# Performance work log

Hardware: AMD Instinct MI355X
Metric: run time of the kernel (lower is better)

Reference implementation:

```python
import jax, jax.numpy as jnp
import numpy as np

V, E, H, B, S, C = 50000, 300, 512, 128, 80, 6
HH = 2 * H  # hidden_dim * num_directions (BiDi=True)


def _gru_dir(x, w_ih, w_hh, b_ih, b_hh, reverse):
    # x: (b, t, e) -> (b, t, h); torch nn.GRU cell math
    Bv, T, _ = x.shape
    Hd = w_hh.shape[1]
    xg = jnp.einsum('bte,ge->btg', x, w_ih) + b_ih  # (b, t, 3h)
    if reverse:
        xg = xg[:, ::-1]
    def step(h, xt):
        gi_r, gi_z, gi_n = jnp.split(xt, 3, axis=-1)
        gh_r, gh_z, gh_n = jnp.split(h @ w_hh.T + b_hh, 3, axis=-1)
        r = jax.nn.sigmoid(gi_r + gh_r)
        z = jax.nn.sigmoid(gi_z + gh_z)
        n = jnp.tanh(gi_n + r * gh_n)
        hn = (1.0 - z) * n + z * h
        return hn, hn
    h0 = jnp.zeros((Bv, Hd), x.dtype)
    _, hs = jax.lax.scan(step, h0, jnp.swapaxes(xg, 0, 1))
    hs = jnp.swapaxes(hs, 0, 1)
    if reverse:
        hs = hs[:, ::-1]
    return hs


def _bigru(x, pf, pb):
    return jnp.concatenate([_gru_dir(x, *pf, reverse=False), _gru_dir(x, *pb, reverse=True)], axis=-1)


def _conv1d(x, w, b, d):
    y = jax.lax.conv_general_dilated(x, w, (1,), 'VALID', rhs_dilation=(d,),
                                     dimension_numbers=('NCH', 'OIH', 'NCH'))
    return y + b[None, :, None]


def _bn(x, g, b, m, v):
    # eval-mode BatchNorm1d with running stats
    return (x - m[None, :, None]) * (g[None, :, None] / jnp.sqrt(v[None, :, None] + 1e-5)) + b[None, :, None]


def setup_inputs():
    key = jax.random.key(0)
    ks = iter(jax.random.split(key, 64))
    def W(*shape):
        return jax.random.normal(next(ks), shape, jnp.float32) * 0.02
    inp = {
        'input_batch': jax.random.randint(next(ks), (B, S), 1, V),
        'choices_batch': jax.random.randint(next(ks), (B, 4, C), 1, V),
        'emb_table': W(V, E),
    }
    for p in ('sg', 'cg'):
        for d in ('f', 'b'):
            inp[p + '_wih_' + d] = W(3 * H, E)
            inp[p + '_whh_' + d] = W(3 * H, H)
            inp[p + '_bih_' + d] = W(3 * H)
            inp[p + '_bhh_' + d] = W(3 * H)
    inp['lin_w'] = W(HH, HH * C)
    inp['lin_b'] = W(HH)
    inp['attn_w'] = W(HH, HH)
    inp['attn_b'] = W(HH)
    inp['c11_w'] = W(HH, S, 3);  inp['c11_b'] = W(HH)
    inp['c13_w'] = W(HH, HH, 3); inp['c13_b'] = W(HH)
    inp['c21_w'] = W(HH, HH, 3); inp['c21_b'] = W(HH)
    inp['c23_w'] = W(HH, HH, 3); inp['c23_b'] = W(HH)
    for i in ('1', '2'):
        inp['bn' + i + '_g'] = jnp.ones((HH,), jnp.float32)
        inp['bn' + i + '_b'] = jnp.zeros((HH,), jnp.float32)
        inp['bn' + i + '_m'] = jnp.zeros((HH,), jnp.float32)
        inp['bn' + i + '_v'] = jnp.ones((HH,), jnp.float32)
    inp['gate_wp'] = W(2 * HH, HH)
    inp['gate_wc'] = W(2 * HH, 2 * HH)
    inp['gate_b'] = W(2 * HH)
    inp['out_wp'] = W(2 * HH, HH)
    inp['out_b'] = W(2 * HH)
    return inp


def reference(input_batch, choices_batch, emb_table,
              sg_wih_f, sg_whh_f, sg_bih_f, sg_bhh_f, sg_wih_b, sg_whh_b, sg_bih_b, sg_bhh_b,
              cg_wih_f, cg_whh_f, cg_bih_f, cg_bhh_f, cg_wih_b, cg_whh_b, cg_bih_b, cg_bhh_b,
              lin_w, lin_b, attn_w, attn_b,
              c11_w, c11_b, c13_w, c13_b, c21_w, c21_b, c23_w, c23_b,
              bn1_g, bn1_b, bn1_m, bn1_v, bn2_g, bn2_b, bn2_m, bn2_v,
              gate_wp, gate_wc, gate_b, out_wp, out_b):
    # --- encode passage: embedding + BiGRU (dropout is eval-mode identity) ---
    sent = _bigru(emb_table[input_batch],
                  (sg_wih_f, sg_whh_f, sg_bih_f, sg_bhh_f),
                  (sg_wih_b, sg_whh_b, sg_bih_b, sg_bhh_b))  # (B, S, 2h)
    cgf = (cg_wih_f, cg_whh_f, cg_bih_f, cg_bhh_f)
    cgb = (cg_wih_b, cg_whh_b, cg_bih_b, cg_bhh_b)

    def choice_vec(tok):  # (B, C) -> (B, 2h)
        g = _bigru(emb_table[tok], cgf, cgb)               # (B, C, 2h)
        return g.reshape(g.shape[0], -1) @ lin_w.T + lin_b

    cvs = [choice_vec(choices_batch[:, i]) for i in range(4)]

    # --- AttnReader: shared Wh/bh, per-choice softmax attention over seq ---
    Wh = jnp.einsum('bsh,hg->bsg', sent, attn_w)  # (B, S, 2h)
    bh = sent @ attn_b                            # (B, S)

    def attn_read(cv):
        a = jax.nn.softmax(jnp.einsum('bsg,bg->bs', Wh, cv) + bh, axis=1)
        return jnp.einsum('bs,bsh->bh', a, sent)  # (B, 2h)

    pars = [attn_read(cv) for cv in cvs]

    # --- IDCNN: Conv1d treats seq dim S as channels (faithful to source) ---
    x = jax.nn.relu(_bn(_conv1d(sent, c11_w, c11_b, 1), bn1_g, bn1_b, bn1_m, bn1_v))
    x = _conv1d(x, c13_w, c13_b, 3)
    x = jax.nn.relu(_bn(_conv1d(x, c21_w, c21_b, 1), bn2_g, bn2_b, bn2_m, bn2_v))
    x = _conv1d(x, c23_w, c23_b, 3)
    P = jnp.max(x, axis=2)  # AdaptiveMaxPool1d(1) + squeeze -> (B, 2h)

    Cs = [jnp.concatenate([cv, par], axis=1) for cv, par in zip(cvs, pars)]  # (B, 4h)

    # --- PointerNet (note: source bug makes out1..out4 all equal C1WP+bC1) ---
    WP = P @ gate_wp.T          # (B, 4h)
    WP_out = P @ out_wp.T       # (B, 4h)
    Cd1 = Cs[0] * jax.nn.sigmoid(WP + Cs[0] @ gate_wc.T + gate_b)
    o1 = jnp.sum(Cd1 * WP_out, axis=1, keepdims=True) + (Cd1 @ out_b)[:, None]  # (B, 1)
    return jnp.concatenate([o1, o1, o1, o1], axis=1)  # (B, 4)
```

## Files before the change

kernel.cpp:

```cpp
#include <hip/hip_runtime.h>

typedef unsigned int u32;
typedef unsigned short u16;
typedef __attribute__((ext_vector_type(4))) float f32x4;
typedef __attribute__((ext_vector_type(8))) short bf16x8;

#define DEV static __device__ __forceinline__

DEV float sigf(float x){ return 1.0f/(1.0f + expf(-x)); }

DEV u16 f2bf(float x){
  u32 u = __float_as_uint(x);
  u32 r = (u + 0x7FFFu + ((u >> 16) & 1u)) >> 16;
  return (u16)r;
}

DEV u32 encf(float f){
  u32 u = __float_as_uint(f);
  return (u & 0x80000000u) ? ~u : (u | 0x80000000u);
}
DEV float decf(u32 e){
  return (e & 0x80000000u) ? __uint_as_float(e ^ 0x80000000u) : __uint_as_float(~e);
}

DEV void gload16(const void* g, void* l){
  __builtin_amdgcn_global_load_lds((const __attribute__((address_space(1))) u32*)g,
                                   (__attribute__((address_space(3))) u32*)l, 16, 0, 0);
}

__global__ __launch_bounds__(256,2) void gemm_bf16(
    const u16* __restrict__ A, const u16* __restrict__ A2,
    const u16* __restrict__ B,
    const float* __restrict__ bias, const float* __restrict__ bias2,
    float* __restrict__ C, float* __restrict__ C2, int ldc,
    int Kp, int ksteps)
{
  __shared__ u16 lds[(128 + 128)*32];
  char* ldsc = (char*)&lds[0];
  const int Boff = 128*64;
  const int tid = threadIdx.x;
  const int l = tid & 63, w = tid >> 6;
  const int n0 = blockIdx.x * 128, m0 = blockIdx.y * 128;
  const u16* Ause = blockIdx.z ? A2 : A;
  const float* buse = blockIdx.z ? bias2 : bias;
  float* Cuse = blockIdx.z ? C2 : C;
  const int wr = w >> 1, wc = w & 1;
  const int lr = l & 15, g = l >> 4;

  f32x4 acc[4][4];
  #pragma unroll
  for (int i=0;i<4;++i)
    #pragma unroll
    for (int j=0;j<4;++j) acc[i][j] = f32x4{0.f,0.f,0.f,0.f};

  for (int ks = 0; ks < ksteps; ++ks) {
    const int i0 = ks*32;
    __syncthreads();
    #pragma unroll
    for (int r = 0; r < 2; ++r) {
      const int rr = w*2 + r;
      const int c = rr*64 + l;
      const int row = c >> 2, bpos = c & 3;
      const int ib = bpos ^ ((row>>1) & 3);
      gload16(Ause + ((size_t)(m0 + row)*Kp + (i0 + ib*8)), ldsc + rr*1024);
      gload16(B    + ((size_t)(n0 + row)*Kp + (i0 + ib*8)), ldsc + Boff + rr*1024);
    }
    __syncthreads();
    bf16x8 af[4], bfr[4];
    #pragma unroll
    for (int m=0;m<4;++m){
      int o = wr*64 + m*16 + lr;
      af[m] = *(const bf16x8*)(ldsc + o*64 + ((g ^ ((o>>1)&3))<<4));
    }
    #pragma unroll
    for (int n=0;n<4;++n){
      int pr = wc*64 + n*16 + lr;
      bfr[n] = *(const bf16x8*)(ldsc + Boff + pr*64 + ((g ^ ((pr>>1)&3))<<4));
    }
    #pragma unroll
    for (int m=0;m<4;++m)
      #pragma unroll
      for (int n=0;n<4;++n)
        acc[m][n] = __builtin_amdgcn_mfma_f32_16x16x32_bf16(af[m], bfr[n], acc[m][n], 0,0,0);
  }

  #pragma unroll
  for (int m=0;m<4;++m){
    int mm = m0 + wr*64 + m*16 + g*4;
    f32x4 bv = *(const f32x4*)(buse + mm);
    #pragma unroll
    for (int n=0;n<4;++n){
      int p = n0 + wc*64 + n*16 + lr;
      f32x4 v;
      #pragma unroll
      for (int r2=0;r2<4;++r2) v[r2] = acc[m][n][r2] + bv[r2];
      *(f32x4*)(Cuse + (size_t)p*ldc + mm) = v;
    }
  }
}

__global__ __launch_bounds__(256,2) void gemm_bf16_sk(
    const u16* __restrict__ A, const u16* __restrict__ B,
    float* __restrict__ C, int ldc, int Kp, int kpc)
{
  __shared__ u16 lds[(128 + 128)*32];
  char* ldsc = (char*)&lds[0];
  const int Boff = 128*64;
  const int tid = threadIdx.x;
  const int l = tid & 63, w = tid >> 6;
  const int n0 = blockIdx.x * 128, m0 = blockIdx.y * 128;
  const int ks0 = blockIdx.z * kpc;
  const int wr = w >> 1, wc = w & 1;
  const int lr = l & 15, g = l >> 4;

  f32x4 acc[4][4];
  #pragma unroll
  for (int i=0;i<4;++i)
    #pragma unroll
    for (int j=0;j<4;++j) acc[i][j] = f32x4{0.f,0.f,0.f,0.f};

  for (int ks = 0; ks < kpc; ++ks) {
    const int i0 = (ks0 + ks)*32;
    __syncthreads();
    #pragma unroll
    for (int r = 0; r < 2; ++r) {
      const int rr = w*2 + r;
      const int c = rr*64 + l;
      const int row = c >> 2, bpos = c & 3;
      const int ib = bpos ^ ((row>>1) & 3);
      gload16(A + ((size_t)(m0 + row)*Kp + (i0 + ib*8)), ldsc + rr*1024);
      gload16(B + ((size_t)(n0 + row)*Kp + (i0 + ib*8)), ldsc + Boff + rr*1024);
    }
    __syncthreads();
    bf16x8 af[4], bfr[4];
    #pragma unroll
    for (int m=0;m<4;++m){
      int o = wr*64 + m*16 + lr;
      af[m] = *(const bf16x8*)(ldsc + o*64 + ((g ^ ((o>>1)&3))<<4));
    }
    #pragma unroll
    for (int n=0;n<4;++n){
      int pr = wc*64 + n*16 + lr;
      bfr[n] = *(const bf16x8*)(ldsc + Boff + pr*64 + ((g ^ ((pr>>1)&3))<<4));
    }
    #pragma unroll
    for (int m=0;m<4;++m)
      #pragma unroll
      for (int n=0;n<4;++n)
        acc[m][n] = __builtin_amdgcn_mfma_f32_16x16x32_bf16(af[m], bfr[n], acc[m][n], 0,0,0);
  }

  #pragma unroll
  for (int m=0;m<4;++m){
    int mm = m0 + wr*64 + m*16 + g*4;
    #pragma unroll
    for (int n=0;n<4;++n){
      int p = n0 + wc*64 + n*16 + lr;
      float* dst = C + (size_t)p*ldc + mm;
      #pragma unroll
      for (int r2=0;r2<4;++r2) atomicAdd(dst + r2, acc[m][n][r2]);
    }
  }
}

__global__ void initc(float* __restrict__ C, const float* __restrict__ bias,
                      int total, int mmask)
{
  int i = blockIdx.x*256 + threadIdx.x;
  if (i < total) C[i] = bias ? bias[i & mmask] : 0.f;
}

__global__ __launch_bounds__(256) void gru_step(
    const float* __restrict__ xg0, const float* __restrict__ xg1,
    const float* __restrict__ whh0, const float* __restrict__ whh1,
    const float* __restrict__ bhh0, const float* __restrict__ bhh1,
    float* __restrict__ hs, int S, int t)
{
  __shared__ float hL[32*520];
  __shared__ float wL[48*132];
  const int tid = threadIdx.x;
  const int tj = tid & 15, tb = tid >> 4;
  const int jg = blockIdx.x;
  const int b0 = blockIdx.y*32;
  const int dir = blockIdx.z;
  const int l = tid & 63, w = tid >> 6;
  const float* xg  = dir ? xg1  : xg0;
  const float* whh = dir ? whh1 : whh0;
  const float* bhh = dir ? bhh1 : bhh0;
  const int tt = dir ? (S-1-t) : t;
  const int j = jg*16 + tj;

  float accr[2], accz[2], accn[2];
  {
    float br = bhh[j], bz = bhh[512+j], bn = bhh[1024+j];
    accr[0]=br; accr[1]=br; accz[0]=bz; accz[1]=bz; accn[0]=bn; accn[1]=bn;
  }

  if (t > 0){
    const int tp = dir ? (tt+1) : (tt-1);
    #pragma unroll
    for (int rr = 0; rr < 8; ++rr){
      int row = w*8 + rr;
      const float* srcb = hs + ((size_t)(b0+row)*S + tp)*1024 + dir*512;
      gload16(srcb + l*4,       (char*)hL + (size_t)(row*520)*4);
      gload16(srcb + 256 + l*4, (char*)hL + (size_t)(row*520 + 256)*4);
    }
    for (int c = 0; c < 4; ++c){
      const int k0 = c*128;
      __syncthreads();
      #pragma unroll
      for (int i = 0; i < 6; ++i){
        int qidx = tid + i*256;
        int row = qidx >> 5, q = qidx & 31;
        int grow = (row>>4)*512 + jg*16 + (row & 15);
        f32x4 v = *(const f32x4*)(whh + (size_t)grow*512 + k0 + q*4);
        *(f32x4*)(wL + row*132 + q*4) = v;
      }
      __syncthreads();
      #pragma unroll 4
      for (int q = 0; q < 32; ++q){
        f32x4 ha  = *(const f32x4*)(hL + (2*tb  )*520 + k0 + q*4);
        f32x4 hb  = *(const f32x4*)(hL + (2*tb+1)*520 + k0 + q*4);
        f32x4 wr4 = *(const f32x4*)(wL + tj*132      + q*4);
        f32x4 wz4 = *(const f32x4*)(wL + (16+tj)*132 + q*4);
        f32x4 wn4 = *(const f32x4*)(wL + (32+tj)*132 + q*4);
        #pragma unroll
        for (int e = 0; e < 4; ++e){
          accr[0] += ha[e]*wr4[e]; accz[0] += ha[e]*wz4[e]; accn[0] += ha[e]*wn4[e];
          accr[1] += hb[e]*wr4[e]; accz[1] += hb[e]*wz4[e]; accn[1] += hb[e]*wn4[e];
        }
      }
    }
  }

  #pragma unroll
  for (int bi = 0; bi < 2; ++bi){
    int lb = 2*tb + bi;
    int b = b0 + lb;
    size_t xbase = ((size_t)b*S + tt)*1536;
    float gir = xg[xbase + j], giz = xg[xbase + 512 + j], gin = xg[xbase + 1024 + j];
    float hp = (t>0) ? hL[lb*520 + j] : 0.f;
    float r = sigf(gir + accr[bi]);
    float z = sigf(giz + accz[bi]);
    float n = tanhf(gin + r*accn[bi]);
    hs[((size_t)b*S + tt)*1024 + dir*512 + j] = (1.f - z)*n + z*hp;
  }
}

__global__ void transpose_sent(const float* __restrict__ sent, u16* __restrict__ sentT)
{
  __shared__ float tl[80][65];
  int b = blockIdx.y, h0 = blockIdx.x*64;
  for (int idx = threadIdx.x; idx < 80*64; idx += 256){
    int s = idx >> 6, hh = idx & 63;
    tl[s][hh] = sent[((size_t)b*80 + s)*1024 + h0 + hh];
  }
  __syncthreads();
  for (int idx = threadIdx.x; idx < 64*96; idx += 256){
    int hh = idx / 96, s = idx % 96;
    sentT[((size_t)b*1024 + h0 + hh)*96 + s] = (s < 80) ? f2bf(tl[s][hh]) : (u16)0;
  }
}

__global__ void attn_scores(const float* __restrict__ sent, const float* __restrict__ u,
                            const float* __restrict__ attn_b, float* __restrict__ sc)
{
  int wid = blockIdx.x*4 + (threadIdx.x >> 6);
  int lane = threadIdx.x & 63;
  const float* row = sent + (size_t)wid*1024;
  const float* ub = u + (size_t)(wid/80)*1024;
  float acc = 0.f;
  for (int h = lane; h < 1024; h += 64) acc += row[h]*(ub[h] + attn_b[h]);
  #pragma unroll
  for (int m = 32; m; m >>= 1) acc += __shfl_xor(acc, m);
  if (lane == 0) sc[wid] = acc;
}

__global__ void softmax80(const float* __restrict__ sc, float* __restrict__ a)
{
  int b = blockIdx.x, l = threadIdx.x;
  float v0 = sc[b*80 + l];
  float v1 = (l < 16) ? sc[b*80 + 64 + l] : -1e30f;
  float mx = fmaxf(v0, v1);
  #pragma unroll
  for (int m = 32; m; m >>= 1) mx = fmaxf(mx, __shfl_xor(mx, m));
  float e0 = expf(v0 - mx);
  float e1 = (l < 16) ? expf(v1 - mx) : 0.f;
  float s = e0 + e1;
  #pragma unroll
  for (int m = 32; m; m >>= 1) s += __shfl_xor(s, m);
  float inv = 1.f/s;
  a[b*80 + l] = e0*inv;
  if (l < 16) a[b*80 + 64 + l] = e1*inv;
}

__global__ void par_cs0(const float* __restrict__ a, const float* __restrict__ sent,
                        const float* __restrict__ cv, float* __restrict__ Cs0)
{
  int b = blockIdx.x;
  for (int h = threadIdx.x; h < 1024; h += 256){
    float acc = 0.f;
    for (int s = 0; s < 80; ++s) acc += a[b*80+s]*sent[((size_t)b*80+s)*1024 + h];
    Cs0[(size_t)b*2048 + 1024 + h] = acc;
    Cs0[(size_t)b*2048 + h] = cv[(size_t)b*1024 + h];
  }
}

__global__ void pack_w8(const float* __restrict__ src, u16* __restrict__ dst,
                        int O, int CIs, int CIp)
{
  int i = blockIdx.x*256 + threadIdx.x;
  int cip8 = CIp >> 3;
  if (i >= 3*O*cip8) return;
  int tap = i/(O*cip8); int rem = i%(O*cip8);
  int o = rem/cip8, cb = (rem%cip8)*8;
  u16 ov[8];
  #pragma unroll
  for (int jj=0;jj<8;++jj){
    int ci = cb + jj;
    ov[jj] = (ci < CIs) ? f2bf(src[((size_t)o*CIs + ci)*3 + tap]) : (u16)0;
  }
  uint4 v;
  v.x = (u32)ov[0] | ((u32)ov[1]<<16);
  v.y = (u32)ov[2] | ((u32)ov[3]<<16);
  v.z = (u32)ov[4] | ((u32)ov[5]<<16);
  v.w = (u32)ov[6] | ((u32)ov[7]<<16);
  *(uint4*)(dst + ((size_t)tap*O + o)*CIp + cb) = v;
}

__global__ void pack_wk8(const float* __restrict__ src, u16* __restrict__ dst,
                         int M, int Ks, int Kp)
{
  int i = blockIdx.x*256 + threadIdx.x;
  int kp8 = Kp >> 3;
  if (i >= M*kp8) return;
  int row = i/kp8, kb = (i%kp8)*8;
  const float* s = src + (size_t)row*Ks + kb;
  u16 ov[8];
  #pragma unroll
  for (int jj=0;jj<8;++jj) ov[jj] = (kb+jj < Ks) ? f2bf(s[jj]) : (u16)0;
  uint4 v;
  v.x = (u32)ov[0] | ((u32)ov[1]<<16);
  v.y = (u32)ov[2] | ((u32)ov[3]<<16);
  v.z = (u32)ov[4] | ((u32)ov[5]<<16);
  v.w = (u32)ov[6] | ((u32)ov[7]<<16);
  *(uint4*)(dst + (size_t)row*Kp + kb) = v;
}

__global__ void pack_f2b8(const float* __restrict__ src, u16* __restrict__ dst, int n)
{
  int i = blockIdx.x*256 + threadIdx.x;
  if (i >= (n>>3)) return;
  const float* s = src + (size_t)i*8;
  uint4 v;
  v.x = (u32)f2bf(s[0]) | ((u32)f2bf(s[1])<<16);
  v.y = (u32)f2bf(s[2]) | ((u32)f2bf(s[3])<<16);
  v.z = (u32)f2bf(s[4]) | ((u32)f2bf(s[5])<<16);
  v.w = (u32)f2bf(s[6]) | ((u32)f2bf(s[7])<<16);
  *(uint4*)(dst + (size_t)i*8) = v;
}

__global__ void pack_x8(const float* __restrict__ emb, const int* __restrict__ toks,
                        int rdiv, int rmul, u16* __restrict__ dst, int R)
{
  int i = blockIdx.x*256 + threadIdx.x;
  if (i >= R*40) return;
  int row = i/40, kb = (i%40)*8;
  int tok = toks[(row/rdiv)*rmul + (row%rdiv)];
  const float* s = emb + (size_t)tok*300 + kb;
  u16 ov[8];
  #pragma unroll
  for (int jj=0;jj<8;++jj) ov[jj] = (kb+jj < 300) ? f2bf(s[jj]) : (u16)0;
  uint4 v;
  v.x = (u32)ov[0] | ((u32)ov[1]<<16);
  v.y = (u32)ov[2] | ((u32)ov[3]<<16);
  v.z = (u32)ov[4] | ((u32)ov[5]<<16);
  v.w = (u32)ov[6] | ((u32)ov[7]<<16);
  *(uint4*)(dst + (size_t)row*320 + kb) = v;
}

__global__ void prep_ab(const float* c11b, const float* c13b, const float* c21b, const float* c23b,
                        const float* g1, const float* b1, const float* m1, const float* v1,
                        const float* g2, const float* b2, const float* m2, const float* v2,
                        float* ab)
{
  int i = blockIdx.x*256 + threadIdx.x;
  if (i >= 4096) return;
  int layer = i >> 10, o = i & 1023;
  float al, be;
  if (layer == 0){ al = g1[o]/sqrtf(v1[o]+1e-5f); be = c11b[o]*al + b1[o] - m1[o]*al; }
  else if (layer == 1){ al = 1.f; be = c13b[o]; }
  else if (layer == 2){ al = g2[o]/sqrtf(v2[o]+1e-5f); be = c21b[o]*al + b2[o] - m2[o]*al; }
  else { al = 1.f; be = c23b[o]; }
  ab[layer*2048 + o] = al;
  ab[layer*2048 + 1024 + o] = be;
}

__global__ void init_penc(u32* p){
  int i = blockIdx.x*256 + threadIdx.x;
  if (i < 128*1024) p[i] = encf(-3.3e38f);
}
__global__ void dec_p(const u32* __restrict__ pe, float* __restrict__ pf){
  int i = blockIdx.x*256 + threadIdx.x;
  if (i < 128*1024) pf[i] = decf(pe[i]);
}

#define CONV_PHASE(TAP, BRD, STAGECODE, WAITCODE)                             \
  {                                                                           \
    const char* Ab = ldsc + (((ks3 + (TAP)) & 3) << 13) + aRd;                \
    const char* Bb = ldsc + 32768 + bpar + (BRD);                             \
    bf16x8 af[8], bfr[4];                                                     \
    _Pragma("unroll")                                                         \
    for (int m=0;m<8;++m) af[m] = *(const bf16x8*)(Ab + m*1024);              \
    _Pragma("unroll")                                                         \
    for (int n=0;n<4;++n) bfr[n] = *(const bf16x8*)(Bb + n*1024);             \
    STAGECODE                                                                 \
    WAITCODE                                                                  \
    __builtin_amdgcn_s_setprio(1);                                            \
    _Pragma("unroll")                                                         \
    for (int n=0;n<4;++n)                                                     \
      _Pragma("unroll")                                                       \
      for (int m=0;m<8;++m)                                                   \
        acc[m][n] = __builtin_amdgcn_mfma_f32_16x16x32_bf16(af[m], bfr[n],    \
                                                            acc[m][n],0,0,0); \
    __builtin_amdgcn_s_setprio(0);                                            \
    asm volatile("" ::: "memory");                                            \
    __builtin_amdgcn_s_barrier();                                             \
    asm volatile("" ::: "memory");                                            \
  }

#define STAGE_A(TAP)                                                          \
      {                                                                       \
        char* Adst = ldsc + (((ks3 + (TAP) + 3) & 3) << 13);                  \
        gload16(aptr0 + (size_t)(TAP)*1024*CI, Adst + aLd0);                  \
        gload16(aptr1 + (size_t)(TAP)*1024*CI, Adst + aLd1);                  \
      }

#define STAGE_B                                                               \
      {                                                                       \
        char* Bdst = ldsc + 32768 + (bpar ^ 17408);                           \
        gload16(bp0, Bdst + bl0);                                             \
        gload16(bp1, Bdst + bl1);                                             \
        gload16(bp2, Bdst + bl2);                                             \
        gload16(bp3, Bdst + bl3);                                             \
        if (l < 16) gload16(bp4, Bdst + bl4);                                 \
      }

__global__ __launch_bounds__(256,2) void conv_mfma(
    const u16* __restrict__ X, long bstrideX,
    const u16* __restrict__ Wt,
    const float* __restrict__ alpha, const float* __restrict__ beta,
    u16* __restrict__ Y, long bstrideY,
    u32* __restrict__ Penc, int b0,
    int P_in, int P_out, int CI, int dil, int ksteps, int mode)
{
  __shared__ u16 lds[33792];
  char* ldsc = (char*)&lds[0];
  const int tid = threadIdx.x;
  const int l = tid & 63, w = tid >> 6;
  const int wg = blockIdx.x + (blockIdx.y<<2) + (blockIdx.z<<5);
  const int id2 = ((wg & 7) << 6) | (wg >> 3);
  const int p0 = (id2 & 3) * 256;
  const int o0 = ((id2 >> 2) & 7) * 128;
  const int bz = id2 >> 5;
  const u16* Xb = X + (size_t)bz * (size_t)bstrideX;
  const int lr = l & 15, g = l >> 4;

  const int aRd  = lr*64 + ((g ^ ((lr>>1)&3))<<4);
  const int bRd0 = (w*64 + lr)*64 + ((g ^ ((lr>>1)&3))<<4);
  const int bRd1 = (w*64 + lr + dil)*64 + ((g ^ (((lr+dil)>>1)&3))<<4);
  const int bRd2 = (w*64 + lr + 2*dil)*64 + ((g ^ (((lr+2*dil)>>1)&3))<<4);

  const u16 *aptr0, *aptr1;
  int aLd0, aLd1;
  {
    int c0 = tid,        r0 = c0 >> 2, i0b = (c0 & 3) ^ ((r0>>1)&3);
    int c1 = 256 + tid,  r1 = c1 >> 2, i1b = (c1 & 3) ^ ((r1>>1)&3);
    aptr0 = Wt + ((size_t)(o0 + r0)*CI + i0b*8);  aLd0 = c0*16;
    aptr1 = Wt + ((size_t)(o0 + r1)*CI + i1b*8);  aLd1 = c1*16;
  }
  const u16 *bp0,*bp1,*bp2,*bp3,*bp4;
  int bl0,bl1,bl2,bl3,bl4;
  {
    const int base = w*272;
#define BSET(PTR, LD, CC)                                                     \
    { int c = (CC); int row = c>>2, bpos = c&3;                               \
      int ib = bpos ^ ((row>>1)&3);                                           \
      int ps = p0 + row; ps = ps < P_in ? ps : (P_in-1);                      \
      PTR = Xb + ((size_t)ps*CI + ib*8);  LD = c*16; }
    BSET(bp0, bl0, base + l)
    BSET(bp1, bl1, base + 64 + l)
    BSET(bp2, bl2, base + 128 + l)
    BSET(bp3, bl3, base + 192 + l)
    BSET(bp4, bl4, base + 256 + (l & 15))
#undef BSET
  }

  f32x4 acc[8][4];
  #pragma unroll
  for (int i=0;i<8;++i)
    #pragma unroll
    for (int j=0;j<4;++j) acc[i][j] = f32x4{0.f,0.f,0.f,0.f};

  {
    gload16(aptr0, ldsc + aLd0);
    gload16(aptr1, ldsc + aLd1);
    gload16(aptr0 + (size_t)1024*CI, ldsc + (1<<13) + aLd0);
    gload16(aptr1 + (size_t)1024*CI, ldsc + (1<<13) + aLd1);
    gload16(aptr0 + (size_t)2048*CI, ldsc + (2<<13) + aLd0);
    gload16(aptr1 + (size_t)2048*CI, ldsc + (2<<13) + aLd1);
    gload16(bp0, ldsc + 32768 + bl0);
    gload16(bp1, ldsc + 32768 + bl1);
    gload16(bp2, ldsc + 32768 + bl2);
    gload16(bp3, ldsc + 32768 + bl3);
    if (l < 16) gload16(bp4, ldsc + 32768 + bl4);
    aptr0 += 32; aptr1 += 32;
    bp0 += 32; bp1 += 32; bp2 += 32; bp3 += 32; bp4 += 32;
  }
  asm volatile("s_waitcnt vmcnt(0)" ::: "memory");
  __builtin_amdgcn_s_barrier();
  asm volatile("" ::: "memory");

  int ks3 = 0;
  for (int ks = 0; ks < ksteps-1; ++ks) {
    const int bpar = (ks & 1) ? 17408 : 0;
    CONV_PHASE(0, bRd0,
      STAGE_A(0) STAGE_B,
      asm volatile("s_waitcnt vmcnt(9)" ::: "memory");)
    CONV_PHASE(1, bRd1,
      STAGE_A(1),
      asm volatile("s_waitcnt vmcnt(9)" ::: "memory");)
    CONV_PHASE(2, bRd2,
      STAGE_A(2)
      { aptr0 += 32; aptr1 += 32;
        bp0 += 32; bp1 += 32; bp2 += 32; bp3 += 32; bp4 += 32; },
      asm volatile("s_waitcnt vmcnt(4)" ::: "memory");)
    ks3 += 3;
  }
  {
    const int bpar = ((ksteps-1) & 1) ? 17408 : 0;
    CONV_PHASE(0, bRd0, {},
      asm volatile("s_waitcnt vmcnt(0)" ::: "memory");)
    CONV_PHASE(1, bRd1, {}, {})
    CONV_PHASE(2, bRd2, {}, {})
  }

  if (mode == 2) {
    #pragma unroll
    for (int m=0;m<8;++m){
      int oo = o0 + m*16 + g*4;
      f32x4 al = *(const f32x4*)(alpha + oo);
      f32x4 be = *(const f32x4*)(beta + oo);
      float vm[4] = {-1e30f,-1e30f,-1e30f,-1e30f};
      #pragma unroll
      for (int n=0;n<4;++n){
        int p = p0 + w*64 + n*16 + lr;
        bool ok = p < P_out;
        #pragma unroll
        for (int r2=0;r2<4;++r2){
          float v = acc[m][n][r2]*al[r2] + be[r2];
          vm[r2] = ok ? fmaxf(vm[r2], v) : vm[r2];
        }
      }
      #pragma unroll
      for (int r2=0;r2<4;++r2){
        float v = vm[r2];
        #pragma unroll
        for (int mask=1; mask<16; mask<<=1) v = fmaxf(v, __shfl_xor(v, mask));
        if (lr == 0) atomicMax(&Penc[(size_t)(b0+bz)*1024 + oo + r2], encf(v));
      }
    }
  } else {
    #pragma unroll
    for (int m=0;m<8;++m){
      int oo = o0 + m*16 + g*4;
      f32x4 al = *(const f32x4*)(alpha + oo);
      f32x4 be = *(const f32x4*)(beta + oo);
      #pragma unroll
      for (int n=0;n<4;++n){
        int p = p0 + w*64 + n*16 + lr;
        if (p < P_out){
          float v0 = acc[m][n][0]*al[0] + be[0];
          float v1 = acc[m][n][1]*al[1] + be[1];
          float v2 = acc[m][n][2]*al[2] + be[2];
          float v3 = acc[m][n][3]*al[3] + be[3];
          if (mode == 0){ v0=fmaxf(v0,0.f); v1=fmaxf(v1,0.f); v2=fmaxf(v2,0.f); v3=fmaxf(v3,0.f); }
          uint2 pk;
          pk.x = (u32)f2bf(v0) | ((u32)f2bf(v1) << 16);
          pk.y = (u32)f2bf(v2) | ((u32)f2bf(v3) << 16);
          *(uint2*)(Y + (size_t)bz*(size_t)bstrideY + (size_t)p*1024 + oo) = pk;
        }
      }
    }
  }
}

__global__ void head_final(const float* __restrict__ Cs0, const float* __restrict__ t1,
                           const float* __restrict__ t2, const float* __restrict__ outb,
                           float* __restrict__ dout)
{
  __shared__ float red[256];
  int b = blockIdx.x;
  float part = 0.f;
  for (int gg = threadIdx.x; gg < 2048; gg += 256){
    float cd = Cs0[(size_t)b*2048+gg] * sigf(t1[(size_t)b*2048+gg]);
    part += cd * (t2[(size_t)b*2048+gg] + outb[gg]);
  }
  red[threadIdx.x] = part;
  __syncthreads();
  for (int s = 128; s > 0; s >>= 1){
    if (threadIdx.x < s) red[threadIdx.x] += red[threadIdx.x + s];
    __syncthreads();
  }
  if (threadIdx.x < 4) dout[b*4 + threadIdx.x] = red[0];
}

extern "C" void kernel_launch(void* const* d_in, const int* in_sizes, int n_in,
                              void* d_out, int out_size, void* d_ws, size_t ws_size,
                              hipStream_t stream)
{
  (void)in_sizes; (void)n_in; (void)out_size; (void)ws_size;
  const int*   input_batch = (const int*)d_in[0];
  const int*   choices     = (const int*)d_in[1];
  const float* emb    = (const float*)d_in[2];
  const float* sgwihf = (const float*)d_in[3];
  const float* sgwhhf = (const float*)d_in[4];
  const float* sgbihf = (const float*)d_in[5];
  const float* sgbhhf = (const float*)d_in[6];
  const float* sgwihb = (const float*)d_in[7];
  const float* sgwhhb = (const float*)d_in[8];
  const float* sgbihb = (const float*)d_in[9];
  const float* sgbhhb = (const float*)d_in[10];
  const float* cgwihf = (const float*)d_in[11];
  const float* cgwhhf = (const float*)d_in[12];
  const float* cgbihf = (const float*)d_in[13];
  const float* cgbhhf = (const float*)d_in[14];
  const float* cgwihb = (const float*)d_in[15];
  const float* cgwhhb = (const float*)d_in[16];
  const float* cgbihb = (const float*)d_in[17];
  const float* cgbhhb = (const float*)d_in[18];
  const float* lin_w  = (const float*)d_in[19];
  const float* lin_b  = (const float*)d_in[20];
  const float* attn_w = (const float*)d_in[21];
  const float* attn_b = (const float*)d_in[22];
  const float* c11w = (const float*)d_in[23];
  const float* c11b = (const float*)d_in[24];
  const float* c13w = (const float*)d_in[25];
  const float* c13b = (const float*)d_in[26];
  const float* c21w = (const float*)d_in[27];
  const float* c21b = (const float*)d_in[28];
  const float* c23w = (const float*)d_in[29];
  const float* c23b = (const float*)d_in[30];
  const float* bn1g = (const float*)d_in[31];
  const float* bn1b = (const float*)d_in[32];
  const float* bn1m = (const float*)d_in[33];
  const float* bn1v = (const float*)d_in[34];
  const float* bn2g = (const float*)d_in[35];
  const float* bn2b = (const float*)d_in[36];
  const float* bn2m = (const float*)d_in[37];
  const float* bn2v = (const float*)d_in[38];
  const float* gatewp = (const float*)d_in[39];
  const float* gatewc = (const float*)d_in[40];
  const float* gateb  = (const float*)d_in[41];
  const float* outwp  = (const float*)d_in[42];
  const float* outb   = (const float*)d_in[43];
  float* dout = (float*)d_out;

  char* ws = (char*)d_ws; size_t off = 0;
  auto alc = [&](size_t n)->char*{ char* p = ws + off; off = (off + n + 255) & ~(size_t)255; return p; };
  float* xg_f  = (float*)alc((size_t)128*80*1536*4);
  float* xg_b  = (float*)alc((size_t)128*80*1536*4);
  float* xg_cf = (float*)alc((size_t)128*6*1536*4);
  float* xg_cb = (float*)alc((size_t)128*6*1536*4);
  float* gh    = (float*)alc((size_t)2*128*1536*4); (void)gh;
  float* sent  = (float*)alc((size_t)128*80*1024*4);
  float* g_c   = (float*)alc((size_t)128*6*1024*4);
  u16*   sentT = (u16*)alc((size_t)128*1024*96*2);
  float* cv    = (float*)alc((size_t)128*1024*4);
  float* uu    = (float*)alc((size_t)128*1024*4);
  float* scb   = (float*)alc((size_t)128*80*4);
  float* aw    = (float*)alc((size_t)128*80*4);
  float* Cs0   = (float*)alc((size_t)128*2048*4);
  u16* W1p = (u16*)alc((size_t)3*1024*96*2);
  u16* W2p = (u16*)alc((size_t)3*1024*1024*2);
  u16* W3p = (u16*)alc((size_t)3*1024*1024*2);
  u16* W4p = (u16*)alc((size_t)3*1024*1024*2);
  float* ab  = (float*)alc((size_t)4*2048*4);
  u32*  Penc = (u32*)alc((size_t)128*1024*4);
  float* Pf  = (float*)alc((size_t)128*1024*4);
  float* t1  = (float*)alc((size_t)128*2048*4);
  float* t2  = (float*)alc((size_t)128*2048*4);
  u16* xbf_s = (u16*)alc((size_t)10240*320*2);
  u16* xbf_c = (u16*)alc((size_t)768*320*2);
  u16* Wsf = (u16*)alc((size_t)1536*320*2);
  u16* Wsb = (u16*)alc((size_t)1536*320*2);
  u16* Wcf = (u16*)alc((size_t)1536*320*2);
  u16* Wcb = (u16*)alc((size_t)1536*320*2);

  char* R1 = (char*)xg_f;
  u16* linw_bf  = (u16*)(R1);
  u16* attnw_bf = (u16*)(R1 + 12582912);
  u16* gcbf     = (u16*)(R1 + 14680064);
  u16* cvbf     = (u16*)(R1 + 16252928);
  const int bc = 16;
  u16* Y0 = (u16*)(R1 + 16515072);
  u16* Y1 = Y0 + (size_t)bc*1024*1024;
  char* R2 = (char*)sent;
  u16* gwp_bf = (u16*)(R2);
  u16* gwc_bf = (u16*)(R2 + 4194304);
  u16* owp_bf = (u16*)(R2 + 12582912);
  u16* Pfbf   = (u16*)(R2 + 16777216);
  u16* Cs0bf  = (u16*)(R2 + 17039360);

  dim3 T(256);

  pack_w8<<<dim3((3*1024*12+255)/256), T, 0, stream>>>(c11w, W1p, 1024, 80, 96);
  pack_w8<<<dim3((3*1024*128+255)/256), T, 0, stream>>>(c13w, W2p, 1024, 1024, 1024);
  pack_w8<<<dim3((3*1024*128+255)/256), T, 0, stream>>>(c21w, W3p, 1024, 1024, 1024);
  pack_w8<<<dim3((3*1024*128+255)/256), T, 0, stream>>>(c23w, W4p, 1024, 1024, 1024);
  pack_wk8<<<dim3((1536*40+255)/256), T, 0, stream>>>(sgwihf, Wsf, 1536, 300, 320);
  pack_wk8<<<dim3((1536*40+255)/256), T, 0, stream>>>(sgwihb, Wsb, 1536, 300, 320);
  pack_wk8<<<dim3((1536*40+255)/256), T, 0, stream>>>(cgwihf, Wcf, 1536, 300, 320);
  pack_wk8<<<dim3((1536*40+255)/256), T, 0, stream>>>(cgwihb, Wcb, 1536, 300, 320);
  pack_x8<<<dim3((10240*40+255)/256), T, 0, stream>>>(emb, input_batch, 80, 80, xbf_s, 10240);
  pack_x8<<<dim3((768*40+255)/256), T, 0, stream>>>(emb, choices, 6, 24, xbf_c, 768);
  prep_ab<<<16, T, 0, stream>>>(c11b, c13b, c21b, c23b,
                                bn1g,bn1b,bn1m,bn1v, bn2g,bn2b,bn2m,bn2v, ab);
  init_penc<<<512, T, 0, stream>>>(Penc);

  gemm_bf16<<<dim3(80,12,2), T, 0, stream>>>(Wsf, Wsb, xbf_s, sgbihf, sgbihb,
                                             xg_f, xg_b, 1536, 320, 10);
  gemm_bf16<<<dim3(6,12,2), T, 0, stream>>>(Wcf, Wcb, xbf_c, cgbihf, cgbihb,
                                            xg_cf, xg_cb, 1536, 320, 10);

  for (int t = 0; t < 80; ++t)
    gru_step<<<dim3(32,4,2), T, 0, stream>>>(xg_f, xg_b, sgwhhf, sgwhhb,
                                             sgbhhf, sgbhhb, sent, 80, t);
  for (int t = 0; t < 6; ++t)
    gru_step<<<dim3(32,4,2), T, 0, stream>>>(xg_cf, xg_cb, cgwhhf, cgwhhb,
                                             cgbhhf, cgbhhb, g_c, 6, t);

  pack_wk8<<<dim3((1024*768+255)/256), T, 0, stream>>>(lin_w, linw_bf, 1024, 6144, 6144);
  pack_wk8<<<dim3((1024*128+255)/256), T, 0, stream>>>(attn_w, attnw_bf, 1024, 1024, 1024);
  pack_f2b8<<<dim3((128*768+255)/256), T, 0, stream>>>(g_c, gcbf, 128*6144);

  transpose_sent<<<dim3(16,128), T, 0, stream>>>(sent, sentT);

  initc<<<dim3((128*1024+255)/256), T, 0, stream>>>(cv, lin_b, 128*1024, 1023);
  gemm_bf16_sk<<<dim3(1,8,6), T, 0, stream>>>(linw_bf, gcbf, cv, 1024, 6144, 32);
  pack_f2b8<<<dim3((128*128+255)/256), T, 0, stream>>>(cv, cvbf, 128*1024);
  initc<<<dim3((128*1024+255)/256), T, 0, stream>>>(uu, nullptr, 128*1024, 1023);
  gemm_bf16_sk<<<dim3(1,8,2), T, 0, stream>>>(attnw_bf, cvbf, uu, 1024, 1024, 16);
  attn_scores<<<2560, T, 0, stream>>>(sent, uu, attn_b, scb);
  softmax80<<<128, dim3(64), 0, stream>>>(scb, aw);
  par_cs0<<<128, T, 0, stream>>>(aw, sent, cv, Cs0);

  pack_wk8<<<dim3((2048*128+255)/256), T, 0, stream>>>(gatewp, gwp_bf, 2048, 1024, 1024);
  pack_wk8<<<dim3((2048*256+255)/256), T, 0, stream>>>(gatewc, gwc_bf, 2048, 2048, 2048);
  pack_wk8<<<dim3((2048*128+255)/256), T, 0, stream>>>(outwp, owp_bf, 2048, 1024, 1024);
  pack_f2b8<<<dim3((128*256+255)/256), T, 0, stream>>>(Cs0, Cs0bf, 128*2048);

  for (int b0 = 0; b0 < 128; b0 += bc){
    conv_mfma<<<dim3(4,8,bc), T, 0, stream>>>(sentT + (size_t)b0*1024*96, (long)1024*96,
        W1p, ab+0,    ab+1024, Y0, (long)1024*1024, nullptr, 0, 1024, 1022, 96,   1, 3,  0);
    conv_mfma<<<dim3(4,8,bc), T, 0, stream>>>(Y0, (long)1024*1024,
        W2p, ab+2048, ab+3072, Y1, (long)1024*1024, nullptr, 0, 1022, 1016, 1024, 3, 32, 1);
    conv_mfma<<<dim3(4,8,bc), T, 0, stream>>>(Y1, (long)1024*1024,
        W3p, ab+4096, ab+5120, Y0, (long)1024*1024, nullptr, 0, 1016, 1014, 1024, 1, 32, 0);
    conv_mfma<<<dim3(4,8,bc), T, 0, stream>>>(Y0, (long)1024*1024,
        W4p, ab+6144, ab+7168, nullptr, 0, Penc, b0,          1014, 1008, 1024, 3, 32, 2);
  }
  dec_p<<<512, T, 0, stream>>>(Penc, Pf);
  pack_f2b8<<<dim3((128*128+255)/256), T, 0, stream>>>(Pf, Pfbf, 128*1024);

  initc<<<dim3((128*2048+255)/256), T, 0, stream>>>(t1, gateb, 128*2048, 2047);
  gemm_bf16_sk<<<dim3(1,16,2), T, 0, stream>>>(gwp_bf, Pfbf, t1, 2048, 1024, 16);
  gemm_bf16_sk<<<dim3(1,16,4), T, 0, stream>>>(gwc_bf, Cs0bf, t1, 2048, 2048, 16);
  initc<<<dim3((128*2048+255)/256), T, 0, stream>>>(t2, nullptr, 128*2048, 2047);
  gemm_bf16_sk<<<dim3(1,16,2), T, 0, stream>>>(owp_bf, Pfbf, t2, 2048, 1024, 16);
  head_final<<<128, T, 0, stream>>>(Cs0, t1, t2, outb, dout);
}
```

Measured before the change: 3.833 ms.

## Move GRU recurrent matmul to bf16 MFMA with packed weights and bf16 hidden buffer

```diff
diff --git a/kernel.cpp b/kernel.cpp
--- a/kernel.cpp
+++ b/kernel.cpp
@@ -170,81 +170,116 @@
   if (i < total) C[i] = bias ? bias[i & mmask] : 0.f;
 }
 
-__global__ __launch_bounds__(256) void gru_step(
+__global__ __launch_bounds__(256) void gru_step_mfma(
     const float* __restrict__ xg0, const float* __restrict__ xg1,
-    const float* __restrict__ whh0, const float* __restrict__ whh1,
+    const u16* __restrict__ Wp0, const u16* __restrict__ Wp1,
     const float* __restrict__ bhh0, const float* __restrict__ bhh1,
-    float* __restrict__ hs, int S, int t)
-{
-  __shared__ float hL[32*520];
-  __shared__ float wL[48*132];
+    float* __restrict__ hs, u16* __restrict__ hbf, int S, int t)
+{
+  __shared__ u16 lds[(192+128)*32];
+  char* ldsc = (char*)&lds[0];
+  const int Boff = 192*64;
   const int tid = threadIdx.x;
-  const int tj = tid & 15, tb = tid >> 4;
-  const int jg = blockIdx.x;
-  const int b0 = blockIdx.y*32;
+  const int l = tid & 63, w = tid >> 6;
+  const int lr = l & 15, g = l >> 4;
+  const int jb = blockIdx.x;
   const int dir = blockIdx.z;
-  const int l = tid & 63, w = tid >> 6;
-  const float* xg  = dir ? xg1  : xg0;
-  const float* whh = dir ? whh1 : whh0;
+  const float* xg  = dir ? xg1 : xg0;
+  const u16*   Wp  = dir ? Wp1 : Wp0;
   const float* bhh = dir ? bhh1 : bhh0;
   const int tt = dir ? (S-1-t) : t;
-  const int j = jg*16 + tj;
-
-  float accr[2], accz[2], accn[2];
-  {
-    float br = bhh[j], bz = bhh[512+j], bn = bhh[1024+j];
-    accr[0]=br; accr[1]=br; accz[0]=bz; accz[1]=bz; accn[0]=bn; accn[1]=bn;
-  }
+
+  f32x4 acc[3][8];
+  #pragma unroll
+  for (int s=0;s<3;++s)
+    #pragma unroll
+    for (int n=0;n<8;++n) acc[s][n] = f32x4{0.f,0.f,0.f,0.f};
 
   if (t > 0){
-    const int tp = dir ? (tt+1) : (tt-1);
-    #pragma unroll
-    for (int rr = 0; rr < 8; ++rr){
-      int row = w*8 + rr;
-      const float* srcb = hs + ((size_t)(b0+row)*S + tp)*1024 + dir*512;
-      gload16(srcb + l*4,       (char*)hL + (size_t)(row*520)*4);
-      gload16(srcb + 256 + l*4, (char*)hL + (size_t)(row*520 + 256)*4);
-    }
-    for (int c = 0; c < 4; ++c){
-      const int k0 = c*128;
+    const u16* RB = hbf + (size_t)((t-1)&1)*131072;
+    const int sw = ((g ^ ((lr>>1)&3))<<4);
+    for (int ks = 0; ks < 16; ++ks){
+      const int i0 = ks*32;
       __syncthreads();
       #pragma unroll
-      for (int i = 0; i < 6; ++i){
-        int qidx = tid + i*256;
-        int row = qidx >> 5, q = qidx & 31;
-        int grow = (row>>4)*512 + jg*16 + (row & 15);
-        f32x4 v = *(const f32x4*)(whh + (size_t)grow*512 + k0 + q*4);
-        *(f32x4*)(wL + row*132 + q*4) = v;
+      for (int r = 0; r < 3; ++r){
+        const int c = r*256 + tid;
+        const int row = c >> 2, bpos = c & 3;
+        const int ib = bpos ^ ((row>>1)&3);
+        gload16(Wp + ((size_t)(jb*192 + row)*512 + i0 + ib*8), ldsc + (size_t)c*16);
+      }
+      #pragma unroll
+      for (int r = 0; r < 2; ++r){
+        const int c = r*256 + tid;
+        const int row = c >> 2, bpos = c & 3;
+        const int ib = bpos ^ ((row>>1)&3);
+        gload16(RB + ((size_t)row*1024 + dir*512 + i0 + ib*8),
+                ldsc + Boff + (size_t)c*16);
       }
       __syncthreads();
-      #pragma unroll 4
-      for (int q = 0; q < 32; ++q){
-        f32x4 ha  = *(const f32x4*)(hL + (2*tb  )*520 + k0 + q*4);
-        f32x4 hb  = *(const f32x4*)(hL + (2*tb+1)*520 + k0 + q*4);
-        f32x4 wr4 = *(const f32x4*)(wL + tj*132      + q*4);
-        f32x4 wz4 = *(const f32x4*)(wL + (16+tj)*132 + q*4);
-        f32x4 wn4 = *(const f32x4*)(wL + (32+tj)*132 + q*4);
+      bf16x8 af[3];
+      #pragma unroll
+      for (int s=0;s<3;++s){
+        int row = (w + 4*s)*16 + lr;
+        af[s] = *(const bf16x8*)(ldsc + row*64 + sw);
+      }
+      #pragma unroll
+      for (int n=0;n<8;++n){
+        int rowb = n*16 + lr;
+        bf16x8 bfr = *(const bf16x8*)(ldsc + Boff + rowb*64 + sw);
         #pragma unroll
-        for (int e = 0; e < 4; ++e){
-          accr[0] += ha[e]*wr4[e]; accz[0] += ha[e]*wz4[e]; accn[0] += ha[e]*wn4[e];
-          accr[1] += hb[e]*wr4[e]; accz[1] += hb[e]*wz4[e]; accn[1] += hb[e]*wn4[e];
-        }
+        for (int s=0;s<3;++s)
+          acc[s][n] = __builtin_amdgcn_mfma_f32_16x16x32_bf16(af[s], bfr, acc[s][n], 0,0,0);
       }
     }
   }
 
-  #pragma unroll
-  for (int bi = 0; bi < 2; ++bi){
-    int lb = 2*tb + bi;
-    int b = b0 + lb;
-    size_t xbase = ((size_t)b*S + tt)*1536;
-    float gir = xg[xbase + j], giz = xg[xbase + 512 + j], gin = xg[xbase + 1024 + j];
-    float hp = (t>0) ? hL[lb*520 + j] : 0.f;
-    float r = sigf(gir + accr[bi]);
-    float z = sigf(giz + accz[bi]);
-    float n = tanhf(gin + r*accn[bi]);
-    hs[((size_t)b*S + tt)*1024 + dir*512 + j] = (1.f - z)*n + z*hp;
-  }
+  const int jj = w*16 + g*4;
+  const int j  = jb*64 + jj;
+  f32x4 bR = *(const f32x4*)(bhh + j);
+  f32x4 bZ = *(const f32x4*)(bhh + 512 + j);
+  f32x4 bN = *(const f32x4*)(bhh + 1024 + j);
+  u16* WB = hbf + (size_t)(t&1)*131072;
+  const int tp = dir ? (tt+1) : (tt-1);
+  #pragma unroll
+  for (int n=0;n<8;++n){
+    int b = n*16 + lr;
+    size_t xb = ((size_t)b*S + tt)*1536 + j;
+    f32x4 gir = *(const f32x4*)(xg + xb);
+    f32x4 giz = *(const f32x4*)(xg + xb + 512);
+    f32x4 gin = *(const f32x4*)(xg + xb + 1024);
+    f32x4 hp = f32x4{0.f,0.f,0.f,0.f};
+    if (t > 0) hp = *(const f32x4*)(hs + ((size_t)b*S + tp)*1024 + dir*512 + j);
+    f32x4 hv;
+    #pragma unroll
+    for (int e=0;e<4;++e){
+      float r = sigf(gir[e] + acc[0][n][e] + bR[e]);
+      float z = sigf(giz[e] + acc[1][n][e] + bZ[e]);
+      float nn = tanhf(gin[e] + r*(acc[2][n][e] + bN[e]));
+      hv[e] = (1.f - z)*nn + z*hp[e];
+    }
+    *(f32x4*)(hs + ((size_t)b*S + tt)*1024 + dir*512 + j) = hv;
+    uint2 pk;
+    pk.x = (u32)f2bf(hv[0]) | ((u32)f2bf(hv[1])<<16);
+    pk.y = (u32)f2bf(hv[2]) | ((u32)f2bf(hv[3])<<16);
+    *(uint2*)(WB + (size_t)b*1024 + dir*512 + j) = pk;
+  }
+}
+
+__global__ void pack_wgru(const float* __restrict__ src, u16* __restrict__ dst)
+{
+  int i = blockIdx.x*256 + threadIdx.x;
+  if (i >= 1536*64) return;
+  int drow = i >> 6, kb = (i & 63)*8;
+  int jb = drow / 192, rr = drow % 192;
+  int gate = rr >> 6, jj = rr & 63;
+  const float* s = src + ((size_t)(gate*512 + jb*64 + jj))*512 + kb;
+  uint4 v;
+  v.x = (u32)f2bf(s[0]) | ((u32)f2bf(s[1])<<16);
+  v.y = (u32)f2bf(s[2]) | ((u32)f2bf(s[3])<<16);
+  v.z = (u32)f2bf(s[4]) | ((u32)f2bf(s[5])<<16);
+  v.w = (u32)f2bf(s[6]) | ((u32)f2bf(s[7])<<16);
+  *(uint4*)(dst + (size_t)drow*512 + kb) = v;
 }
 
 __global__ void transpose_sent(const float* __restrict__ sent, u16* __restrict__ sentT)
@@ -711,6 +746,11 @@
   u16* owp_bf = (u16*)(R2 + 12582912);
   u16* Pfbf   = (u16*)(R2 + 16777216);
   u16* Cs0bf  = (u16*)(R2 + 17039360);
+  u16* Wpsf = sentT;
+  u16* Wpsb = sentT +  786432;
+  u16* Wpcf = sentT + 1572864;
+  u16* Wpcb = sentT + 2359296;
+  u16* hbf  = sentT + 3145728;
 
   dim3 T(256);
 
@@ -724,6 +764,10 @@
   pack_wk8<<<dim3((1536*40+255)/256), T, 0, stream>>>(cgwihb, Wcb, 1536, 300, 320);
   pack_x8<<<dim3((10240*40+255)/256), T, 0, stream>>>(emb, input_batch, 80, 80, xbf_s, 10240);
   pack_x8<<<dim3((768*40+255)/256), T, 0, stream>>>(emb, choices, 6, 24, xbf_c, 768);
+  pack_wgru<<<dim3(384), T, 0, stream>>>(sgwhhf, Wpsf);
+  pack_wgru<<<dim3(384), T, 0, stream>>>(sgwhhb, Wpsb);
+  pack_wgru<<<dim3(384), T, 0, stream>>>(cgwhhf, Wpcf);
+  pack_wgru<<<dim3(384), T, 0, stream>>>(cgwhhb, Wpcb);
   prep_ab<<<16, T, 0, stream>>>(c11b, c13b, c21b, c23b,
                                 bn1g,bn1b,bn1m,bn1v, bn2g,bn2b,bn2m,bn2v, ab);
   init_penc<<<512, T, 0, stream>>>(Penc);
@@ -734,11 +778,11 @@
                                             xg_cf, xg_cb, 1536, 320, 10);
 
   for (int t = 0; t < 80; ++t)
-    gru_step<<<dim3(32,4,2), T, 0, stream>>>(xg_f, xg_b, sgwhhf, sgwhhb,
-                                             sgbhhf, sgbhhb, sent, 80, t);
+    gru_step_mfma<<<dim3(8,1,2), T, 0, stream>>>(xg_f, xg_b, Wpsf, Wpsb,
+                                                 sgbhhf, sgbhhb, sent, hbf, 80, t);
   for (int t = 0; t < 6; ++t)
-    gru_step<<<dim3(32,4,2), T, 0, stream>>>(xg_cf, xg_cb, cgwhhf, cgwhhb,
-                                             cgbhhf, cgbhhb, g_c, 6, t);
+    gru_step_mfma<<<dim3(8,1,2), T, 0, stream>>>(xg_cf, xg_cb, Wpcf, Wpcb,
+                                                 cgbhhf, cgbhhb, g_c, hbf, 6, t);
 
   pack_wk8<<<dim3((1024*768+255)/256), T, 0, stream>>>(lin_w, linw_bf, 1024, 6144, 6144);
   pack_wk8<<<dim3((1024*128+255)/256), T, 0, stream>>>(attn_w, attnw_bf, 1024, 1024, 1024);
```

Measured after the change: 4.789 ms. 24.9% more time.
